# Optimization experiments

Hardware: AMD Instinct MI355X
Metric: run time of the kernel (lower is better)

Reference implementation:

```python
import jax, jax.numpy as jnp
import numpy as np

TOP_K = 90
TEMP = 0.04
EPS_LN = 1e-5

def _l2norm(x):
    n = jnp.linalg.norm(x, axis=-1, keepdims=True)
    return x / jnp.maximum(n, 1e-12)

def _layernorm(x, g, b):
    mu = jnp.mean(x, axis=-1, keepdims=True)
    var = jnp.mean((x - mu) ** 2, axis=-1, keepdims=True)
    return (x - mu) * jax.lax.rsqrt(var + EPS_LN) * g + b

def setup_inputs() -> dict:
    key = jax.random.key(0)
    ks = jax.random.split(key, 8)
    B, N, D, ES = 2048, 100000, 1024, 101
    H1, H2 = 256, 128
    inp = {
        "en_1024": jax.random.normal(ks[0], (B, D), jnp.float32),
        "en_db": jax.random.normal(ks[1], (N, D), jnp.float32),
        "es_db": jax.random.normal(ks[2], (N, D), jnp.float32),
        "sp_idx": jax.random.randint(ks[3], (ES,), 0, D),
        "W1": jax.random.normal(ks[4], (D + ES, H1), jnp.float32) * 0.02,
        "b1": jnp.zeros((H1,), jnp.float32),
        "g1": jnp.ones((H1,), jnp.float32),
        "be1": jnp.zeros((H1,), jnp.float32),
        "W2": jax.random.normal(ks[5], (H1, H2), jnp.float32) * 0.02,
        "b2": jnp.zeros((H2,), jnp.float32),
        "g2": jnp.ones((H2,), jnp.float32),
        "be2": jnp.zeros((H2,), jnp.float32),
        "W3": jax.random.normal(ks[6], (H2, ES), jnp.float32) * 0.02,
        "b3": jnp.zeros((ES,), jnp.float32),
    }
    return inp

def reference(en_1024, en_db, es_db, sp_idx, W1, b1, g1, be1, W2, b2, g2, be2, W3, b3):
    # --- retrieval: cosine sim + topk softmax + weighted gather-sum ---
    q = _l2norm(en_1024)            # (B, 1024)
    db = _l2norm(en_db)             # (N, 1024)
    sims = q @ db.T                 # (B, N)
    top_sims, top_idx = jax.lax.top_k(sims, TOP_K)      # (B, K)
    w = jax.nn.softmax(top_sims / TEMP, axis=-1)        # (B, K)
    gathered = es_db[top_idx]       # (B, K, 1024)
    es_retrieved_1024 = jnp.einsum('bk,bkd->bd', w, gathered)  # (B, 1024)
    es_retrieved_101 = es_retrieved_1024[:, sp_idx]     # (B, 101)
    # --- fusion MLP (residual correction) ---
    feat = jnp.concatenate([en_1024, es_retrieved_101], axis=-1)  # (B, 1125)
    h = jax.nn.gelu(_layernorm(feat @ W1 + b1, g1, be1), approximate=False)
    h = jax.nn.gelu(_layernorm(h @ W2 + b2, g2, be2), approximate=False)
    delta = h @ W3 + b3
    es_pred_101 = es_retrieved_101 + delta
    return (es_pred_101, es_retrieved_101, delta)
```

## Files before the change

### kernel.cpp

```cpp
#include <hip/hip_runtime.h>
#include <hip/hip_bf16.h>
#include <hip/hip_fp16.h>

typedef int i32x4 __attribute__((ext_vector_type(4)));
typedef float f32x4 __attribute__((ext_vector_type(4)));

#define B_ROWS 2048
#define N_DB   100000
#define D_DIM  1024
#define ES     101
#define H1D    256
#define H2D    128
#define TOPK   90
#define TKEEP  128
#define TEMPV  0.04f
#define NTOT   100352
#define NT_ALL 392
#define ESS    104
#define CAP    1024
#define CNTS   16
#define RCAP   24
#define GTHR   0.085f

#define GLOAD16(g, l) __builtin_amdgcn_global_load_lds( \
    (const __attribute__((address_space(1))) unsigned int*)(g), \
    (__attribute__((address_space(3))) unsigned int*)(l), 16, 0, 0)

__device__ inline int q8clamp(float x) {
  int q = (int)rintf(x);
  return q < -127 ? -127 : (q > 127 ? 127 : q);
}

__global__ __launch_bounds__(256) void qnorm_kernel(const float* __restrict__ en,
                                                    char* __restrict__ qa,
                                                    float* __restrict__ fa) {
  __shared__ float red[4], redm[4];
  int b = blockIdx.x, t = threadIdx.x;
  float4 v = ((const float4*)(en + (size_t)b * D_DIM))[t];
  float ss = v.x * v.x + v.y * v.y + v.z * v.z + v.w * v.w;
  float mx = fmaxf(fmaxf(fabsf(v.x), fabsf(v.y)), fmaxf(fabsf(v.z), fabsf(v.w)));
  for (int o = 32; o; o >>= 1) { ss += __shfl_xor(ss, o); mx = fmaxf(mx, __shfl_xor(mx, o)); }
  if ((t & 63) == 0) { red[t >> 6] = ss; redm[t >> 6] = mx; }
  __syncthreads();
  float tot = red[0] + red[1] + red[2] + red[3];
  float mtot = fmaxf(fmaxf(redm[0], redm[1]), fmaxf(redm[2], redm[3]));
  float s = fmaxf(mtot, 1e-30f) / 127.0f;
  float rs = 1.0f / s;
  if (t == 0) fa[b] = s / fmaxf(sqrtf(tot), 1e-12f);
  int packed = (q8clamp(v.x * rs) & 0xff) | ((q8clamp(v.y * rs) & 0xff) << 8) |
               ((q8clamp(v.z * rs) & 0xff) << 16) | ((q8clamp(v.w * rs) & 0xff) << 24);
  ((int*)(qa + (size_t)b * D_DIM))[t] = packed;
}

__global__ __launch_bounds__(64) void qat_kernel(const char* __restrict__ qa,
                                                 char* __restrict__ qaT) {
  int m = blockIdx.x, c = threadIdx.x;
  int kb = c >> 3, s = (c >> 2) & 1, l4 = c & 3;
  int g = m >> 4, l15 = m & 15;
  const int4 v = *(const int4*)(qa + (size_t)m * D_DIM + c * 16);
  *(int4*)(qaT + (size_t)g * 16384 + kb * 2048 + s * 1024 + l15 * 64 + l4 * 16) = v;
}

__global__ __launch_bounds__(256) void prep_kernel(const float* __restrict__ db,
                                                   char* __restrict__ qb,
                                                   float* __restrict__ fb,
                                                   const float* __restrict__ es,
                                                   const int* __restrict__ sp,
                                                   float* __restrict__ es_sub) {
  __shared__ float red[4], redm[4];
  __shared__ float row[1024];
  __shared__ int sps[ES];
  int r = blockIdx.x, t = threadIdx.x;
  if (r >= N_DB) {
    ((int*)(qb + (size_t)r * D_DIM))[t] = 0;
    if (t == 0) fb[r] = 0.f;
    return;
  }
  float4 v = ((const float4*)(db + (size_t)r * D_DIM))[t];
  float ss = v.x * v.x + v.y * v.y + v.z * v.z + v.w * v.w;
  float mx = fmaxf(fmaxf(fabsf(v.x), fabsf(v.y)), fmaxf(fabsf(v.z), fabsf(v.w)));
  for (int o = 32; o; o >>= 1) { ss += __shfl_xor(ss, o); mx = fmaxf(mx, __shfl_xor(mx, o)); }
  if ((t & 63) == 0) { red[t >> 6] = ss; redm[t >> 6] = mx; }
  if (t < ES) sps[t] = sp[t];
  ((float4*)row)[t] = ((const float4*)(es + (size_t)r * D_DIM))[t];
  __syncthreads();
  float tot = red[0] + red[1] + red[2] + red[3];
  float mtot = fmaxf(fmaxf(redm[0], redm[1]), fmaxf(redm[2], redm[3]));
  float s = fmaxf(mtot, 1e-30f) / 127.0f;
  float rs = 1.0f / s;
  if (t == 0) fb[r] = s / fmaxf(sqrtf(tot), 1e-12f);
  int packed = (q8clamp(v.x * rs) & 0xff) | ((q8clamp(v.y * rs) & 0xff) << 8) |
               ((q8clamp(v.z * rs) & 0xff) << 16) | ((q8clamp(v.w * rs) & 0xff) << 24);
  ((int*)(qb + (size_t)r * D_DIM))[t] = packed;
  if (t < ES) es_sub[(size_t)r * ESS + t] = row[sps[t]];
}

__global__ __launch_bounds__(512) void gemm_kernel(const char* __restrict__ qaT,
                                                   const char* __restrict__ qb,
                                                   const float* __restrict__ fav,
                                                   const float* __restrict__ fbv,
                                                   float* __restrict__ cand_v,
                                                   int* __restrict__ cand_i,
                                                   int* __restrict__ cand_cnt) {
  __shared__ char shmem[52224];
  char* Bs = shmem;
  int t = threadIdx.x;
  int lane = t & 63, wid = t >> 6;
  int wr = wid >> 2, wc = wid & 3;
  int l15 = lane & 15, l4 = lane >> 4;
  int id = blockIdx.x;
  int swz = (id & 7) * (gridDim.x >> 3) + (id >> 3);
  int bm = swz & 7, bn = swz >> 3;
  int m0 = bm * 256;
  int col0 = bn * 256;

  const char* srcB[4];
  int dstoff[4];
  #pragma unroll
  for (int i = 0; i < 4; ++i) {
    int L = i * 512 + t;
    int row = L >> 3;
    int colb = ((L & 7) * 16) ^ ((row & 7) << 4);
    srcB[i] = qb + (size_t)(col0 + row) * D_DIM + colb;
    dstoff[i] = L * 16;
  }
  const char* aptr[8];
  int aoff = l15 * 64 + l4 * 16;
  #pragma unroll
  for (int f = 0; f < 8; ++f)
    aptr[f] = qaT + (size_t)(bm * 16 + wr * 8 + f) * 16384 + aoff;

  i32x4 acc[8][4] = {};

  for (int kt = 0; kt < D_DIM; kt += 128) {
    int kb2 = (kt >> 7) * 2048;
    i32x4 a[8][2];
    #pragma unroll
    for (int f = 0; f < 8; ++f) {
      a[f][0] = *(const i32x4*)(aptr[f] + kb2);
      a[f][1] = *(const i32x4*)(aptr[f] + kb2 + 1024);
    }
    #pragma unroll
    for (int i = 0; i < 4; ++i) GLOAD16(srcB[i] + kt, Bs + dstoff[i]);
    __syncthreads();
    #pragma unroll
    for (int s = 0; s < 2; ++s) {
      i32x4 b[4];
      #pragma unroll
      for (int f = 0; f < 4; ++f) {
        int rowB = wc * 64 + f * 16 + l15;
        int offB = rowB * 128 + ((s * 64 + l4 * 16) ^ ((rowB & 7) << 4));
        b[f] = *(const i32x4*)(Bs + offB);
      }
      #pragma unroll
      for (int fm = 0; fm < 8; ++fm)
        #pragma unroll
        for (int fn = 0; fn < 4; ++fn)
          acc[fm][fn] = __builtin_amdgcn_mfma_i32_16x16x64_i8(a[fm][s], b[fn], acc[fm][fn], 0, 0, 0);
    }
    __syncthreads();
  }

  float*    fa_l = (float*)shmem;
  float*    fb_l = (float*)(shmem + 1024);
  unsigned* rcnt = (unsigned*)(shmem + 2048);
  float*    rvv  = (float*)(shmem + 3072);
  int*      rvi  = (int*)(shmem + 27648);
  if (t < 256) {
    fa_l[t] = fav[m0 + t];
    fb_l[t] = (col0 + t < N_DB) ? fbv[col0 + t] : 0.f;
    rcnt[t] = 0;
  }
  __syncthreads();
  #pragma unroll
  for (int fm = 0; fm < 8; ++fm)
    #pragma unroll
    for (int fn = 0; fn < 4; ++fn) {
      int ncl = wc * 64 + fn * 16 + l15;
      int gcol = col0 + ncl;
      if (gcol >= N_DB) continue;
      float fbn = fb_l[ncl];
      #pragma unroll
      for (int r = 0; r < 4; ++r) {
        int lrow = wr * 128 + fm * 16 + l4 * 4 + r;
        float v = (float)acc[fm][fn][r] * fa_l[lrow] * fbn;
        if (v > GTHR) {
          unsigned p = atomicAdd(&rcnt[lrow], 1u);
          if (p < RCAP) { rvv[lrow * RCAP + p] = v; rvi[lrow * RCAP + p] = gcol; }
        }
      }
    }
  __syncthreads();
  if (t < 256) {
    unsigned k = rcnt[t]; if (k > RCAP) k = RCAP;
    if (k) {
      int m = m0 + t;
      int base = atomicAdd(&cand_cnt[(size_t)m * CNTS], (int)k);
      for (unsigned j = 0; j < k; ++j) {
        int p = base + (int)j;
        if (p < CAP) {
          cand_v[(size_t)m * CAP + p] = rvv[t * RCAP + j];
          cand_i[(size_t)m * CAP + p] = rvi[t * RCAP + j];
        }
      }
    }
  }
}

__device__ inline void bsort(float* cv, int* ci, int t, int cnt, int p2) {
  for (int i = t; i < p2; i += 256)
    if (i >= cnt) { cv[i] = -3e38f; ci[i] = 0x7fffffff; }
  for (int k = 2; k <= p2; k <<= 1)
    for (int j = k >> 1; j > 0; j >>= 1) {
      __syncthreads();
      for (int i = t; i < p2; i += 256) {
        int ixj = i ^ j;
        if (ixj > i) {
          float v1 = cv[i], v2 = cv[ixj];
          int i1 = ci[i], i2 = ci[ixj];
          bool aBeforeB = (v1 > v2) || (v1 == v2 && i1 < i2);
          bool dirAsc = (i & k) != 0;
          bool doSwap = dirAsc ? aBeforeB : !aBeforeB;
          if (doSwap) { cv[i] = v2; cv[ixj] = v1; ci[i] = i2; ci[ixj] = i1; }
        }
      }
    }
  __syncthreads();
}

__global__ __launch_bounds__(256) void select_rescore_kernel(const float* __restrict__ cand_v,
                                                             const int* __restrict__ cand_i,
                                                             const int* __restrict__ cand_cnt,
                                                             const float* __restrict__ en,
                                                             const float* __restrict__ db,
                                                             const float* __restrict__ es_sub,
                                                             float* __restrict__ esr,
                                                             float* __restrict__ out_esr) {
  __shared__ float cv[CAP];
  __shared__ int   ci[CAP];
  __shared__ float qs[1024];
  __shared__ double wred[4];
  __shared__ float w[TOPK];
  __shared__ float ssum;
  int b = blockIdx.x, t = threadIdx.x;
  int lane = t & 63, wid = t >> 6;
  int nc = cand_cnt[(size_t)b * CNTS]; if (nc > CAP) nc = CAP;
  for (int i = t; i < nc; i += 256) {
    cv[i] = cand_v[(size_t)b * CAP + i];
    ci[i] = cand_i[(size_t)b * CAP + i];
  }
  double nq2 = 0.0;
  for (int i = t; i < 1024; i += 256) {
    float v = en[(size_t)b * D_DIM + i];
    qs[i] = v;
    nq2 = fma((double)v, (double)v, nq2);
  }
  for (int o = 32; o; o >>= 1) nq2 += __shfl_xor(nq2, o);
  if (lane == 0) wred[wid] = nq2;
  __syncthreads();
  int p2 = 128; while (p2 < nc) p2 <<= 1;
  bsort(cv, ci, t, nc, p2);
  double nq2t = wred[0] + wred[1] + wred[2] + wred[3];
  double nq = sqrt(nq2t); if (nq < 1e-12) nq = 1e-12;
  const f32x4* qs4 = (const f32x4*)qs;
  for (int c = wid * 32; c < wid * 32 + 32; ++c) {
    int idx = ci[c];
    if (idx < 0 || idx >= N_DB) idx = 0;
    const f32x4* dr4 = (const f32x4*)(db + (size_t)idx * D_DIM);
    double dot = 0.0, nd2 = 0.0;
    #pragma unroll
    for (int j = 0; j < 4; ++j) {
      f32x4 d = dr4[lane + j * 64];
      f32x4 q = qs4[lane + j * 64];
      #pragma unroll
      for (int e = 0; e < 4; ++e) {
        dot = fma((double)q[e], (double)d[e], dot);
        nd2 = fma((double)d[e], (double)d[e], nd2);
      }
    }
    for (int o = 32; o; o >>= 1) { dot += __shfl_xor(dot, o); nd2 += __shfl_xor(nd2, o); }
    if (lane == 0) {
      double nd = sqrt(nd2); if (nd < 1e-12) nd = 1e-12;
      cv[c] = (float)(dot / (nq * nd));
      ci[c] = idx;
    }
  }
  __syncthreads();
  bsort(cv, ci, t, TKEEP, TKEEP);
  if (t < TOPK) w[t] = expf((cv[t] - cv[0]) / TEMPV);
  __syncthreads();
  if (t == 0) {
    float s = 0.f;
    for (int k = 0; k < TOPK; ++k) s += w[k];
    ssum = s;
  }
  __syncthreads();
  float inv = 1.0f / ssum;
  if (t < ES) {
    float acc = 0.f;
    for (int k = 0; k < TOPK; ++k) acc += w[k] * es_sub[(size_t)ci[k] * ESS + t];
    acc *= inv;
    esr[b * ES + t] = acc;
    out_esr[b * ES + t] = acc;
  }
}

__global__ __launch_bounds__(256) void mlp_kernel(const float* __restrict__ en,
                                                  const float* __restrict__ esr,
                                                  const float* __restrict__ W1, const float* __restrict__ b1,
                                                  const float* __restrict__ g1, const float* __restrict__ be1,
                                                  const float* __restrict__ W2, const float* __restrict__ b2,
                                                  const float* __restrict__ g2, const float* __restrict__ be2,
                                                  const float* __restrict__ W3, const float* __restrict__ b3,
                                                  float* __restrict__ out) {
  __shared__ float feat[8][1128];
  __shared__ float h1s[8][H1D];
  __shared__ float h2s[8][H2D];
  int t = threadIdx.x;
  int b0 = blockIdx.x * 8;
  int wid = t >> 6, lane = t & 63;
  for (int r = 0; r < 8; ++r) {
    const float* src = en + (size_t)(b0 + r) * D_DIM;
    for (int i = t; i < 1024; i += 256) feat[r][i] = src[i];
    if (t < ES) feat[r][1024 + t] = esr[(b0 + r) * ES + t];
  }
  __syncthreads();
  float acc[8];
  #pragma unroll
  for (int r = 0; r < 8; ++r) acc[r] = b1[t];
  for (int k = 0; k < 1125; ++k) {
    float wv = W1[k * H1D + t];
    #pragma unroll
    for (int r = 0; r < 8; ++r) acc[r] += feat[r][k] * wv;
  }
  #pragma unroll
  for (int r = 0; r < 8; ++r) h1s[r][t] = acc[r];
  __syncthreads();
  for (int rr = 0; rr < 2; ++rr) {
    int r = wid + rr * 4;
    float s = 0.f, s2 = 0.f;
    for (int j = lane; j < H1D; j += 64) { float x = h1s[r][j]; s += x; s2 += x * x; }
    for (int o = 32; o; o >>= 1) { s += __shfl_xor(s, o); s2 += __shfl_xor(s2, o); }
    float mu = s / H1D, var = s2 / H1D - mu * mu, rs = rsqrtf(var + 1e-5f);
    for (int j = lane; j < H1D; j += 64) {
      float x = (h1s[r][j] - mu) * rs * g1[j] + be1[j];
      h1s[r][j] = 0.5f * x * (1.0f + erff(x * 0.70710678118654752f));
    }
  }
  __syncthreads();
  if (t < H2D) {
    float acc2[8];
    #pragma unroll
    for (int r = 0; r < 8; ++r) acc2[r] = b2[t];
    for (int k = 0; k < H1D; ++k) {
      float wv = W2[k * H2D + t];
      #pragma unroll
      for (int r = 0; r < 8; ++r) acc2[r] += h1s[r][k] * wv;
    }
    #pragma unroll
    for (int r = 0; r < 8; ++r) h2s[r][t] = acc2[r];
  }
  __syncthreads();
  for (int rr = 0; rr < 2; ++rr) {
    int r = wid + rr * 4;
    float s = 0.f, s2 = 0.f;
    for (int j = lane; j < H2D; j += 64) { float x = h2s[r][j]; s += x; s2 += x * x; }
    for (int o = 32; o; o >>= 1) { s += __shfl_xor(s, o); s2 += __shfl_xor(s2, o); }
    float mu = s / H2D, var = s2 / H2D - mu * mu, rs = rsqrtf(var + 1e-5f);
    for (int j = lane; j < H2D; j += 64) {
      float x = (h2s[r][j] - mu) * rs * g2[j] + be2[j];
      h2s[r][j] = 0.5f * x * (1.0f + erff(x * 0.70710678118654752f));
    }
  }
  __syncthreads();
  if (t < ES) {
    for (int r = 0; r < 8; ++r) {
      float a = b3[t];
      for (int k = 0; k < H2D; ++k) a += h2s[r][k] * W3[k * ES + t];
      float ev = esr[(b0 + r) * ES + t];
      out[(size_t)(b0 + r) * ES + t] = ev + a;
      out[2 * (size_t)B_ROWS * ES + (size_t)(b0 + r) * ES + t] = a;
    }
  }
}

extern "C" void kernel_launch(void* const* d_in, const int* in_sizes, int n_in,
                              void* d_out, int out_size, void* d_ws, size_t ws_size,
                              hipStream_t stream) {
  const float* en   = (const float*)d_in[0];
  const float* endb = (const float*)d_in[1];
  const float* esdb = (const float*)d_in[2];
  const int*   sp   = (const int*)d_in[3];
  const float* W1   = (const float*)d_in[4];
  const float* b1   = (const float*)d_in[5];
  const float* g1   = (const float*)d_in[6];
  const float* be1  = (const float*)d_in[7];
  const float* W2   = (const float*)d_in[8];
  const float* b2   = (const float*)d_in[9];
  const float* g2   = (const float*)d_in[10];
  const float* be2  = (const float*)d_in[11];
  const float* W3   = (const float*)d_in[12];
  const float* b3   = (const float*)d_in[13];
  float* out = (float*)d_out;

  char* ws = (char*)d_ws;
  size_t off = 0;
  auto alloc = [&](size_t bytes) -> void* {
    void* p = ws + off;
    off += (bytes + 255) & ~(size_t)255;
    return p;
  };
  char*  qa     = (char*) alloc((size_t)B_ROWS * D_DIM);
  char*  qaT    = (char*) alloc((size_t)B_ROWS * D_DIM);
  char*  qb     = (char*) alloc((size_t)NTOT * D_DIM);
  float* fa     = (float*)alloc((size_t)B_ROWS * sizeof(float));
  float* fb     = (float*)alloc((size_t)NTOT * sizeof(float));
  float* cand_v = (float*)alloc((size_t)B_ROWS * CAP * sizeof(float));
  int*   cand_i = (int*)  alloc((size_t)B_ROWS * CAP * sizeof(int));
  int*   cand_cnt = (int*)alloc((size_t)B_ROWS * CNTS * sizeof(int));
  float* es_sub = (float*)alloc((size_t)N_DB * ESS * sizeof(float));
  float* esr    = (float*)alloc((size_t)B_ROWS * ES * sizeof(float));
  (void)ws_size; (void)in_sizes; (void)n_in; (void)out_size;

  hipMemsetAsync(cand_cnt, 0, (size_t)B_ROWS * CNTS * sizeof(int), stream);
  hipLaunchKernelGGL(qnorm_kernel, dim3(B_ROWS), dim3(256), 0, stream, en, qa, fa);
  hipLaunchKernelGGL(qat_kernel, dim3(B_ROWS), dim3(64), 0, stream, qa, qaT);
  hipLaunchKernelGGL(prep_kernel, dim3(NTOT), dim3(256), 0, stream, endb, qb, fb, esdb, sp, es_sub);
  hipLaunchKernelGGL(gemm_kernel, dim3(NT_ALL * 8), dim3(512), 0, stream,
                     qaT, qb, fa, fb, cand_v, cand_i, cand_cnt);
  hipLaunchKernelGGL(select_rescore_kernel, dim3(B_ROWS), dim3(256), 0, stream,
                     cand_v, cand_i, cand_cnt, en, endb, es_sub,
                     esr, out + (size_t)B_ROWS * ES);
  hipLaunchKernelGGL(mlp_kernel, dim3(B_ROWS / 8), dim3(256), 0, stream,
                     en, esr, W1, b1, g1, be1, W2, b2, g2, be2, W3, b3, out);
}
```

Before: 1.003 ms.

## Store quantized A and B in MFMA fragment layout and load B directly

The quantize kernels now write int8 rows straight into the MFMA fragment-packed layout, which removes the separate qat transpose kernel. The database operand is packed the same way, so the GEMM loads B fragments directly from global memory into registers. This drops the LDS staging through global_load_lds and both per-iteration __syncthreads. In exchange, B reuse across the waves in a block now goes through cache instead of LDS, and prep_kernel does scattered 4-byte stores.

New measurement: 1.021 ms. About the same (+1.8%).

```diff
diff --git a/kernel.cpp b/kernel.cpp
--- a/kernel.cpp
+++ b/kernel.cpp
@@ -22,17 +22,20 @@
 #define RCAP   24
 #define GTHR   0.085f
 
-#define GLOAD16(g, l) __builtin_amdgcn_global_load_lds( \
-    (const __attribute__((address_space(1))) unsigned int*)(g), \
-    (__attribute__((address_space(3))) unsigned int*)(l), 16, 0, 0)
-
 __device__ inline int q8clamp(float x) {
   int q = (int)rintf(x);
   return q < -127 ? -127 : (q > 127 ? 127 : q);
 }
 
+__device__ inline size_t frag_addr(int m, int t) {
+  int g = m >> 4, l15 = m & 15;
+  int c = t >> 2;
+  int kb = c >> 3, s = (c >> 2) & 1, l4 = c & 3;
+  return (size_t)g * 16384 + kb * 2048 + s * 1024 + l15 * 64 + l4 * 16 + (t & 3) * 4;
+}
+
 __global__ __launch_bounds__(256) void qnorm_kernel(const float* __restrict__ en,
-                                                    char* __restrict__ qa,
+                                                    char* __restrict__ qaT,
                                                     float* __restrict__ fa) {
   __shared__ float red[4], redm[4];
   int b = blockIdx.x, t = threadIdx.x;
@@ -49,20 +52,11 @@
   if (t == 0) fa[b] = s / fmaxf(sqrtf(tot), 1e-12f);
   int packed = (q8clamp(v.x * rs) & 0xff) | ((q8clamp(v.y * rs) & 0xff) << 8) |
                ((q8clamp(v.z * rs) & 0xff) << 16) | ((q8clamp(v.w * rs) & 0xff) << 24);
-  ((int*)(qa + (size_t)b * D_DIM))[t] = packed;
-}
-
-__global__ __launch_bounds__(64) void qat_kernel(const char* __restrict__ qa,
-                                                 char* __restrict__ qaT) {
-  int m = blockIdx.x, c = threadIdx.x;
-  int kb = c >> 3, s = (c >> 2) & 1, l4 = c & 3;
-  int g = m >> 4, l15 = m & 15;
-  const int4 v = *(const int4*)(qa + (size_t)m * D_DIM + c * 16);
-  *(int4*)(qaT + (size_t)g * 16384 + kb * 2048 + s * 1024 + l15 * 64 + l4 * 16) = v;
+  *(int*)(qaT + frag_addr(b, t)) = packed;
 }
 
 __global__ __launch_bounds__(256) void prep_kernel(const float* __restrict__ db,
-                                                   char* __restrict__ qb,
+                                                   char* __restrict__ qbT,
                                                    float* __restrict__ fb,
                                                    const float* __restrict__ es,
                                                    const int* __restrict__ sp,
@@ -72,7 +66,7 @@
   __shared__ int sps[ES];
   int r = blockIdx.x, t = threadIdx.x;
   if (r >= N_DB) {
-    ((int*)(qb + (size_t)r * D_DIM))[t] = 0;
+    *(int*)(qbT + frag_addr(r, t)) = 0;
     if (t == 0) fb[r] = 0.f;
     return;
   }
@@ -91,19 +85,18 @@
   if (t == 0) fb[r] = s / fmaxf(sqrtf(tot), 1e-12f);
   int packed = (q8clamp(v.x * rs) & 0xff) | ((q8clamp(v.y * rs) & 0xff) << 8) |
                ((q8clamp(v.z * rs) & 0xff) << 16) | ((q8clamp(v.w * rs) & 0xff) << 24);
-  ((int*)(qb + (size_t)r * D_DIM))[t] = packed;
+  *(int*)(qbT + frag_addr(r, t)) = packed;
   if (t < ES) es_sub[(size_t)r * ESS + t] = row[sps[t]];
 }
 
 __global__ __launch_bounds__(512) void gemm_kernel(const char* __restrict__ qaT,
-                                                   const char* __restrict__ qb,
+                                                   const char* __restrict__ qbT,
                                                    const float* __restrict__ fav,
                                                    const float* __restrict__ fbv,
                                                    float* __restrict__ cand_v,
                                                    int* __restrict__ cand_i,
                                                    int* __restrict__ cand_cnt) {
   __shared__ char shmem[52224];
-  char* Bs = shmem;
   int t = threadIdx.x;
   int lane = t & 63, wid = t >> 6;
   int wr = wid >> 2, wc = wid & 3;
@@ -114,51 +107,33 @@
   int m0 = bm * 256;
   int col0 = bn * 256;
 
-  const char* srcB[4];
-  int dstoff[4];
-  #pragma unroll
-  for (int i = 0; i < 4; ++i) {
-    int L = i * 512 + t;
-    int row = L >> 3;
-    int colb = ((L & 7) * 16) ^ ((row & 7) << 4);
-    srcB[i] = qb + (size_t)(col0 + row) * D_DIM + colb;
-    dstoff[i] = L * 16;
-  }
-  const char* aptr[8];
   int aoff = l15 * 64 + l4 * 16;
-  #pragma unroll
-  for (int f = 0; f < 8; ++f)
-    aptr[f] = qaT + (size_t)(bm * 16 + wr * 8 + f) * 16384 + aoff;
+  const char* aB = qaT + (size_t)(bm * 16 + wr * 8) * 16384 + aoff;
+  const char* bB = qbT + (size_t)(bn * 16 + wc * 4) * 16384 + aoff;
 
   i32x4 acc[8][4] = {};
 
-  for (int kt = 0; kt < D_DIM; kt += 128) {
-    int kb2 = (kt >> 7) * 2048;
-    i32x4 a[8][2];
+  #pragma unroll 1
+  for (int kt = 0; kt < 8; ++kt) {
+    int o = kt * 2048;
+    i32x4 a[8][2], b[4][2];
     #pragma unroll
     for (int f = 0; f < 8; ++f) {
-      a[f][0] = *(const i32x4*)(aptr[f] + kb2);
-      a[f][1] = *(const i32x4*)(aptr[f] + kb2 + 1024);
-    }
-    #pragma unroll
-    for (int i = 0; i < 4; ++i) GLOAD16(srcB[i] + kt, Bs + dstoff[i]);
-    __syncthreads();
-    #pragma unroll
-    for (int s = 0; s < 2; ++s) {
-      i32x4 b[4];
-      #pragma unroll
-      for (int f = 0; f < 4; ++f) {
-        int rowB = wc * 64 + f * 16 + l15;
-        int offB = rowB * 128 + ((s * 64 + l4 * 16) ^ ((rowB & 7) << 4));
-        b[f] = *(const i32x4*)(Bs + offB);
-      }
+      a[f][0] = *(const i32x4*)(aB + (size_t)f * 16384 + o);
+      a[f][1] = *(const i32x4*)(aB + (size_t)f * 16384 + o + 1024);
+    }
+    #pragma unroll
+    for (int f = 0; f < 4; ++f) {
+      b[f][0] = *(const i32x4*)(bB + (size_t)f * 16384 + o);
+      b[f][1] = *(const i32x4*)(bB + (size_t)f * 16384 + o + 1024);
+    }
+    #pragma unroll
+    for (int s = 0; s < 2; ++s)
       #pragma unroll
       for (int fm = 0; fm < 8; ++fm)
         #pragma unroll
         for (int fn = 0; fn < 4; ++fn)
-          acc[fm][fn] = __builtin_amdgcn_mfma_i32_16x16x64_i8(a[fm][s], b[fn], acc[fm][fn], 0, 0, 0);
-    }
-    __syncthreads();
+          acc[fm][fn] = __builtin_amdgcn_mfma_i32_16x16x64_i8(a[fm][s], b[fn][s], acc[fm][fn], 0, 0, 0);
   }
 
   float*    fa_l = (float*)shmem;
@@ -410,9 +385,8 @@
     off += (bytes + 255) & ~(size_t)255;
     return p;
   };
-  char*  qa     = (char*) alloc((size_t)B_ROWS * D_DIM);
   char*  qaT    = (char*) alloc((size_t)B_ROWS * D_DIM);
-  char*  qb     = (char*) alloc((size_t)NTOT * D_DIM);
+  char*  qbT    = (char*) alloc((size_t)NTOT * D_DIM);
   float* fa     = (float*)alloc((size_t)B_ROWS * sizeof(float));
   float* fb     = (float*)alloc((size_t)NTOT * sizeof(float));
   float* cand_v = (float*)alloc((size_t)B_ROWS * CAP * sizeof(float));
@@ -423,11 +397,10 @@
   (void)ws_size; (void)in_sizes; (void)n_in; (void)out_size;
 
   hipMemsetAsync(cand_cnt, 0, (size_t)B_ROWS * CNTS * sizeof(int), stream);
-  hipLaunchKernelGGL(qnorm_kernel, dim3(B_ROWS), dim3(256), 0, stream, en, qa, fa);
-  hipLaunchKernelGGL(qat_kernel, dim3(B_ROWS), dim3(64), 0, stream, qa, qaT);
-  hipLaunchKernelGGL(prep_kernel, dim3(NTOT), dim3(256), 0, stream, endb, qb, fb, esdb, sp, es_sub);
+  hipLaunchKernelGGL(qnorm_kernel, dim3(B_ROWS), dim3(256), 0, stream, en, qaT, fa);
+  hipLaunchKernelGGL(prep_kernel, dim3(NTOT), dim3(256), 0, stream, endb, qbT, fb, esdb, sp, es_sub);
   hipLaunchKernelGGL(gemm_kernel, dim3(NT_ALL * 8), dim3(512), 0, stream,
-                     qaT, qb, fa, fb, cand_v, cand_i, cand_cnt);
+                     qaT, qbT, fa, fb, cand_v, cand_i, cand_cnt);
   hipLaunchKernelGGL(select_rescore_kernel, dim3(B_ROWS), dim3(256), 0, stream,
                      cand_v, cand_i, cand_cnt, en, endb, es_sub,
                      esr, out + (size_t)B_ROWS * ES);
```

## Stage A tile through LDS in int8 GEMM and shrink block to 256x128

Applied to the files above, without the earlier changes.

The GEMM no longer reads a pre-transposed A operand directly from global memory into registers. It stages the A tile into swizzled LDS with global_load_lds, the same way as B, which removes the separate qat transpose kernel and its buffer. Block tiles shrink from 256x256 with 512 threads to 256x128 with 256 threads, doubling the grid; the epilogue shared-memory layout is adjusted to match. In exchange, each block now fetches more A data per unit of output and the kernel depends more on LDS bandwidth.

Measured after the change: 1.120 ms. 11.7% more time.

```diff
diff --git a/kernel.cpp b/kernel.cpp
--- a/kernel.cpp
+++ b/kernel.cpp
@@ -15,7 +15,7 @@
 #define TKEEP  128
 #define TEMPV  0.04f
 #define NTOT   100352
-#define NT_ALL 392
+#define NT128  784
 #define ESS    104
 #define CAP    1024
 #define CNTS   16
@@ -50,15 +50,6 @@
   int packed = (q8clamp(v.x * rs) & 0xff) | ((q8clamp(v.y * rs) & 0xff) << 8) |
                ((q8clamp(v.z * rs) & 0xff) << 16) | ((q8clamp(v.w * rs) & 0xff) << 24);
   ((int*)(qa + (size_t)b * D_DIM))[t] = packed;
-}
-
-__global__ __launch_bounds__(64) void qat_kernel(const char* __restrict__ qa,
-                                                 char* __restrict__ qaT) {
-  int m = blockIdx.x, c = threadIdx.x;
-  int kb = c >> 3, s = (c >> 2) & 1, l4 = c & 3;
-  int g = m >> 4, l15 = m & 15;
-  const int4 v = *(const int4*)(qa + (size_t)m * D_DIM + c * 16);
-  *(int4*)(qaT + (size_t)g * 16384 + kb * 2048 + s * 1024 + l15 * 64 + l4 * 16) = v;
 }
 
 __global__ __launch_bounds__(256) void prep_kernel(const float* __restrict__ db,
@@ -95,7 +86,7 @@
   if (t < ES) es_sub[(size_t)r * ESS + t] = row[sps[t]];
 }
 
-__global__ __launch_bounds__(512) void gemm_kernel(const char* __restrict__ qaT,
+__global__ __launch_bounds__(256) void gemm_kernel(const char* __restrict__ qa,
                                                    const char* __restrict__ qb,
                                                    const float* __restrict__ fav,
                                                    const float* __restrict__ fbv,
@@ -104,48 +95,53 @@
                                                    int* __restrict__ cand_cnt) {
   __shared__ char shmem[52224];
   char* Bs = shmem;
+  char* As = shmem + 16384;
   int t = threadIdx.x;
   int lane = t & 63, wid = t >> 6;
-  int wr = wid >> 2, wc = wid & 3;
+  int wr = wid >> 1, wc = wid & 1;
   int l15 = lane & 15, l4 = lane >> 4;
   int id = blockIdx.x;
   int swz = (id & 7) * (gridDim.x >> 3) + (id >> 3);
   int bm = swz & 7, bn = swz >> 3;
   int m0 = bm * 256;
-  int col0 = bn * 256;
-
-  const char* srcB[4];
-  int dstoff[4];
+  int col0 = bn * 128;
+
+  const char* srcA[8]; int dstA[8];
+  #pragma unroll
+  for (int i = 0; i < 8; ++i) {
+    int L = i * 256 + t;
+    int row = L >> 3;
+    int colb = ((L & 7) * 16) ^ ((row & 7) << 4);
+    srcA[i] = qa + (size_t)(m0 + row) * D_DIM + colb;
+    dstA[i] = L * 16;
+  }
+  const char* srcB[4]; int dstB[4];
   #pragma unroll
   for (int i = 0; i < 4; ++i) {
-    int L = i * 512 + t;
+    int L = i * 256 + t;
     int row = L >> 3;
     int colb = ((L & 7) * 16) ^ ((row & 7) << 4);
     srcB[i] = qb + (size_t)(col0 + row) * D_DIM + colb;
-    dstoff[i] = L * 16;
-  }
-  const char* aptr[8];
-  int aoff = l15 * 64 + l4 * 16;
-  #pragma unroll
-  for (int f = 0; f < 8; ++f)
-    aptr[f] = qaT + (size_t)(bm * 16 + wr * 8 + f) * 16384 + aoff;
+    dstB[i] = L * 16;
+  }
 
   i32x4 acc[8][4] = {};
 
   for (int kt = 0; kt < D_DIM; kt += 128) {
-    int kb2 = (kt >> 7) * 2048;
-    i32x4 a[8][2];
-    #pragma unroll
-    for (int f = 0; f < 8; ++f) {
-      a[f][0] = *(const i32x4*)(aptr[f] + kb2);
-      a[f][1] = *(const i32x4*)(aptr[f] + kb2 + 1024);
-    }
-    #pragma unroll
-    for (int i = 0; i < 4; ++i) GLOAD16(srcB[i] + kt, Bs + dstoff[i]);
+    #pragma unroll
+    for (int i = 0; i < 8; ++i) GLOAD16(srcA[i] + kt, As + dstA[i]);
+    #pragma unroll
+    for (int i = 0; i < 4; ++i) GLOAD16(srcB[i] + kt, Bs + dstB[i]);
     __syncthreads();
     #pragma unroll
     for (int s = 0; s < 2; ++s) {
-      i32x4 b[4];
+      i32x4 a[8], b[4];
+      #pragma unroll
+      for (int f = 0; f < 8; ++f) {
+        int rowA = wr * 128 + f * 16 + l15;
+        int offA = rowA * 128 + ((s * 64 + l4 * 16) ^ ((rowA & 7) << 4));
+        a[f] = *(const i32x4*)(As + offA);
+      }
       #pragma unroll
       for (int f = 0; f < 4; ++f) {
         int rowB = wc * 64 + f * 16 + l15;
@@ -156,21 +152,18 @@
       for (int fm = 0; fm < 8; ++fm)
         #pragma unroll
         for (int fn = 0; fn < 4; ++fn)
-          acc[fm][fn] = __builtin_amdgcn_mfma_i32_16x16x64_i8(a[fm][s], b[fn], acc[fm][fn], 0, 0, 0);
+          acc[fm][fn] = __builtin_amdgcn_mfma_i32_16x16x64_i8(a[fm], b[fn], acc[fm][fn], 0, 0, 0);
     }
     __syncthreads();
   }
 
   float*    fa_l = (float*)shmem;
   float*    fb_l = (float*)(shmem + 1024);
-  unsigned* rcnt = (unsigned*)(shmem + 2048);
-  float*    rvv  = (float*)(shmem + 3072);
-  int*      rvi  = (int*)(shmem + 27648);
-  if (t < 256) {
-    fa_l[t] = fav[m0 + t];
-    fb_l[t] = (col0 + t < N_DB) ? fbv[col0 + t] : 0.f;
-    rcnt[t] = 0;
-  }
+  unsigned* rcnt = (unsigned*)(shmem + 1536);
+  float*    rvv  = (float*)(shmem + 2560);
+  int*      rvi  = (int*)(shmem + 27136);
+  if (t < 256) { fa_l[t] = fav[m0 + t]; rcnt[t] = 0; }
+  if (t < 128) fb_l[t] = (col0 + t < N_DB) ? fbv[col0 + t] : 0.f;
   __syncthreads();
   #pragma unroll
   for (int fm = 0; fm < 8; ++fm)
@@ -411,7 +404,6 @@
     return p;
   };
   char*  qa     = (char*) alloc((size_t)B_ROWS * D_DIM);
-  char*  qaT    = (char*) alloc((size_t)B_ROWS * D_DIM);
   char*  qb     = (char*) alloc((size_t)NTOT * D_DIM);
   float* fa     = (float*)alloc((size_t)B_ROWS * sizeof(float));
   float* fb     = (float*)alloc((size_t)NTOT * sizeof(float));
@@ -424,10 +416,9 @@
 
   hipMemsetAsync(cand_cnt, 0, (size_t)B_ROWS * CNTS * sizeof(int), stream);
   hipLaunchKernelGGL(qnorm_kernel, dim3(B_ROWS), dim3(256), 0, stream, en, qa, fa);
-  hipLaunchKernelGGL(qat_kernel, dim3(B_ROWS), dim3(64), 0, stream, qa, qaT);
   hipLaunchKernelGGL(prep_kernel, dim3(NTOT), dim3(256), 0, stream, endb, qb, fb, esdb, sp, es_sub);
-  hipLaunchKernelGGL(gemm_kernel, dim3(NT_ALL * 8), dim3(512), 0, stream,
-                     qaT, qb, fa, fb, cand_v, cand_i, cand_cnt);
+  hipLaunchKernelGGL(gemm_kernel, dim3(NT128 * 8), dim3(256), 0, stream,
+                     qa, qb, fa, fb, cand_v, cand_i, cand_cnt);
   hipLaunchKernelGGL(select_rescore_kernel, dim3(B_ROWS), dim3(256), 0, stream,
                      cand_v, cand_i, cand_cnt, en, endb, es_sub,
                      esr, out + (size_t)B_ROWS * ES);
```
